# Kernel optimization log

Measured on AMD Instinct MI355X. Metric: run time of the kernel, lower is better.

The kernel has to match this reference:

```python
import jax, jax.numpy as jnp
import numpy as np

B, D_IN, H, D_OUT = 1024, 64, 128, 16


def setup_inputs() -> dict:
    key = jax.random.key(0)
    k0, k1, k2 = jax.random.split(key, 3)
    x = jax.random.normal(k0, (B, D_IN), dtype=jnp.float32)
    W1 = jax.random.normal(k1, (D_IN, H), dtype=jnp.float32) / np.sqrt(D_IN).astype(np.float32)
    b1 = jnp.zeros((H,), dtype=jnp.float32)
    W2 = jax.random.normal(k2, (H, D_OUT), dtype=jnp.float32) / np.sqrt(H).astype(np.float32)
    b2 = jnp.zeros((D_OUT,), dtype=jnp.float32)
    return {"x": x, "W1": W1, "b1": b1, "W2": W2, "b2": b2}


def reference(x, W1, b1, W2, b2):
    # Wrapped net: 2-layer tanh MLP (hessQuik NN equivalent).
    def f_single(xi):  # xi: [D_IN] -> [D_OUT]
        return jnp.tanh(xi @ W1 + b1) @ W2 + b2

    # f: [B, D_OUT]  (torch: f.view(B, -1))
    f = jax.vmap(f_single)(x)

    # Torch builds df[b, i, j] = d f_j / d x_i via one grad per output column;
    # one reverse sweep per output == jacrev, vmapped over batch.
    J = jax.vmap(jax.jacrev(f_single))(x)            # [B, D_OUT, D_IN]
    df = jnp.transpose(J, (0, 2, 1))                 # [B, D_IN, D_OUT]

    # Torch builds d2f[b, k, i, j] = d^2 f_j / (d x_k d x_i); symmetric in (k, i).
    Hs = jax.vmap(jax.hessian(f_single))(x)          # [B, D_OUT, D_IN, D_IN]
    d2f = jnp.transpose(Hs, (0, 2, 3, 1))            # [B, D_IN, D_IN, D_OUT]

    return f, df, d2f
```

## Files before the change

### kernel.cpp

```cpp
#include <hip/hip_runtime.h>
#include <hip/hip_bf16.h>


typedef unsigned short u16;
typedef short s8v __attribute__((ext_vector_type(8)));
typedef float f4v __attribute__((ext_vector_type(4)));

__device__ __forceinline__ u16 f2bf(float f){
  __hip_bfloat16 h = __float2bfloat16(f);
  return __builtin_bit_cast(u16, h);
}

#define W1S 132

__global__ __launch_bounds__(256) void k2_fused(
    const float* __restrict__ x, const float* __restrict__ W1, const float* __restrict__ b1,
    const float* __restrict__ W2, float* __restrict__ d2f)
{
  const int tid  = threadIdx.x;
  const int lane = tid & 63;
  const int wave = tid >> 6;
  const int n = lane & 15;
  const int q = lane >> 4;
  const int b0 = blockIdx.x * 4;
  const int mb = blockIdx.y;

  __shared__ float sW1[64 * W1S];
  __shared__ u16   sG[4 * 2048];
  __shared__ float sx[256];

#pragma unroll
  for (int v = 0; v < 8; ++v){
    int idx = v*256 + tid;
    int r = idx >> 5;
    int c = (idx & 31) << 2;
    *(f4v*)&sW1[r*W1S + c] = *(const f4v*)&W1[r*128 + c];
  }
  sx[tid] = x[b0*64 + tid];
  __syncthreads();

#pragma unroll
  for (int it = 0; it < 2; ++it){
    int idx = it*256 + tid;
    int s = idx >> 7;
    int h = idx & 127;
    float z = b1[h];
#pragma unroll 8
    for (int i = 0; i < 64; ++i) z += sx[s*64 + i] * sW1[i*W1S + h];
    float a = tanhf(z);
    float t = -2.0f * a * (1.0f - a*a);
    f4v w2r[4];
#pragma unroll
    for (int v2 = 0; v2 < 4; ++v2) w2r[v2] = *(const f4v*)&W2[h*16 + v2*4];
#pragma unroll
    for (int j = 0; j < 16; ++j){
      int byte = (j*256 + h*2) ^ ((j & 7) << 4);
      sG[s*2048 + (byte >> 1)] = f2bf(t * w2r[j >> 2][j & 3]);
    }
  }
  __syncthreads();

  s8v bfrag[4][4];
#pragma unroll
  for (int s = 0; s < 4; ++s){
#pragma unroll
    for (int ks = 0; ks < 4; ++ks){
      int byte = (n*256 + q*16 + ks*64) ^ ((n & 7) << 4);
      bfrag[s][ks] = *(const s8v*)&sG[s*2048 + (byte >> 1)];
    }
  }

  const int R0 = mb*2048 + wave*512;
#pragma unroll 2
  for (int mt = 0; mt < 32; ++mt){
    const int rowbase = R0 + mt*16;
    const int r = rowbase + n;
    const int i = r & 63;
    const int k = r >> 6;
    const float* wi = &sW1[i*W1S];
    const float* wk = &sW1[k*W1S];
    s8v afrag[4];
#pragma unroll
    for (int ks = 0; ks < 4; ++ks){
      int c = q*8 + ks*32;
      f4v ia = *(const f4v*)&wi[c];
      f4v ib = *(const f4v*)&wi[c+4];
      f4v ka = *(const f4v*)&wk[c];
      f4v kb = *(const f4v*)&wk[c+4];
      s8v av;
#pragma unroll
      for (int e = 0; e < 4; ++e) av[e]   = (short)f2bf(ia[e]*ka[e]);
#pragma unroll
      for (int e = 0; e < 4; ++e) av[4+e] = (short)f2bf(ib[e]*kb[e]);
      afrag[ks] = av;
    }
#pragma unroll
    for (int s = 0; s < 4; ++s){
      f4v acc = {0.f, 0.f, 0.f, 0.f};
#pragma unroll
      for (int ks = 0; ks < 4; ++ks)
        acc = __builtin_amdgcn_mfma_f32_16x16x32_bf16(bfrag[s][ks], afrag[ks], acc, 0, 0, 0);
      float* op = d2f + (size_t)(b0 + s)*65536 + (size_t)(rowbase + n)*16 + q*4;
      __builtin_nontemporal_store(acc, (f4v*)op);
    }
  }
}

__global__ __launch_bounds__(128) void k1_fdf(
    const float* __restrict__ x,  const float* __restrict__ W1, const float* __restrict__ b1,
    const float* __restrict__ W2, const float* __restrict__ b2,
    float* __restrict__ f_out, float* __restrict__ df_out)
{
  const int b   = blockIdx.x;
  const int tid = threadIdx.x;

  __shared__ float sx[64];
  __shared__ float s_a[128];
  __shared__ float s_sw2[128 * 16];

  if (tid < 64) sx[tid] = x[b*64 + tid];
  __syncthreads();

  float z = b1[tid];
#pragma unroll 8
  for (int i = 0; i < 64; ++i) z += sx[i] * W1[i*128 + tid];
  float a = tanhf(z);
  float s = 1.0f - a*a;
  s_a[tid] = a;
#pragma unroll
  for (int j = 0; j < 16; ++j)
    s_sw2[tid*16 + j] = s * W2[tid*16 + j];
  __syncthreads();

  if (tid < 16){
    float acc = b2[tid];
    for (int h = 0; h < 128; ++h) acc += s_a[h] * W2[h*16 + tid];
    __builtin_nontemporal_store(acc, &f_out[b*16 + tid]);
  }

  const int i  = tid >> 1;
  const int j0 = (tid & 1) * 8;
  float acc[8] = {0,0,0,0,0,0,0,0};
  for (int h0 = 0; h0 < 128; h0 += 8){
    const float4* wp = (const float4*)&W1[i*128 + h0];
    float4 wa = wp[0], wb = wp[1];
    float wf[8] = {wa.x, wa.y, wa.z, wa.w, wb.x, wb.y, wb.z, wb.w};
#pragma unroll
    for (int hh = 0; hh < 8; ++hh){
      const float4* sp = (const float4*)&s_sw2[(h0 + hh)*16 + j0];
      float4 A = sp[0], Bv = sp[1];
      float w1 = wf[hh];
      acc[0] += w1*A.x;  acc[1] += w1*A.y;  acc[2] += w1*A.z;  acc[3] += w1*A.w;
      acc[4] += w1*Bv.x; acc[5] += w1*Bv.y; acc[6] += w1*Bv.z; acc[7] += w1*Bv.w;
    }
  }
  f4v v0 = {acc[0], acc[1], acc[2], acc[3]};
  f4v v1 = {acc[4], acc[5], acc[6], acc[7]};
  float* dp = &df_out[b*1024 + i*16 + j0];
  __builtin_nontemporal_store(v0, (f4v*)dp);
  __builtin_nontemporal_store(v1, (f4v*)(dp + 4));
}

extern "C" void kernel_launch(void* const* d_in, const int* in_sizes, int n_in,
                              void* d_out, int out_size, void* d_ws, size_t ws_size,
                              hipStream_t stream)
{
  (void)in_sizes; (void)n_in; (void)out_size; (void)d_ws; (void)ws_size;
  const float* x  = (const float*)d_in[0];
  const float* W1 = (const float*)d_in[1];
  const float* b1 = (const float*)d_in[2];
  const float* W2 = (const float*)d_in[3];
  const float* b2 = (const float*)d_in[4];

  float* out     = (float*)d_out;
  float* f_out   = out;
  float* df_out  = out + 16384;
  float* d2f_out = out + 1064960;

  k2_fused<<<dim3(256, 2), 256, 0, stream>>>(x, W1, b1, W2, d2f_out);
  k1_fdf<<<1024, 128, 0, stream>>>(x, W1, b1, W2, b2, f_out, df_out);
}
```

Before: 298.9 us.

## Fuse f/df computation into the Hessian kernel and drop the second launch

Merges the separate f/df kernel into the d2f kernel. Each (batch-group, half) block reuses the tanh values it already computed for two of its four samples to produce f and df, staging s*W2 in the now-freed Hessian LDS buffer. This removes one kernel launch and recomputation of the hidden layer. It adds an extra barrier and some serial work before the MFMA store loop. The d2f stores also change from nontemporal to regular stores.

Result: faster. 276.3 us (-7.5%).

```diff
diff --git a/kernel.cpp b/kernel.cpp
--- a/kernel.cpp
+++ b/kernel.cpp
@@ -13,9 +13,10 @@
 
 #define W1S 132
 
-__global__ __launch_bounds__(256) void k2_fused(
+__global__ __launch_bounds__(256) void k_all(
     const float* __restrict__ x, const float* __restrict__ W1, const float* __restrict__ b1,
-    const float* __restrict__ W2, float* __restrict__ d2f)
+    const float* __restrict__ W2, const float* __restrict__ b2,
+    float* __restrict__ f_out, float* __restrict__ df_out, float* __restrict__ d2f)
 {
   const int tid  = threadIdx.x;
   const int lane = tid & 63;
@@ -26,8 +27,9 @@
   const int mb = blockIdx.y;
 
   __shared__ float sW1[64 * W1S];
-  __shared__ u16   sG[4 * 2048];
+  __shared__ __align__(16) float sGF[4096];
   __shared__ float sx[256];
+  u16* sG = (u16*)sGF;
 
 #pragma unroll
   for (int v = 0; v < 8; ++v){
@@ -39,6 +41,7 @@
   sx[tid] = x[b0*64 + tid];
   __syncthreads();
 
+  float a_keep = 0.f, s_keep = 0.f;
 #pragma unroll
   for (int it = 0; it < 2; ++it){
     int idx = it*256 + tid;
@@ -48,7 +51,9 @@
 #pragma unroll 8
     for (int i = 0; i < 64; ++i) z += sx[s*64 + i] * sW1[i*W1S + h];
     float a = tanhf(z);
-    float t = -2.0f * a * (1.0f - a*a);
+    float sd = 1.0f - a*a;
+    float t = -2.0f * a * sd;
+    if (it == mb){ a_keep = a; s_keep = sd; }
     f4v w2r[4];
 #pragma unroll
     for (int v2 = 0; v2 < 4; ++v2) w2r[v2] = *(const f4v*)&W2[h*16 + v2*4];
@@ -67,6 +72,55 @@
     for (int ks = 0; ks < 4; ++ks){
       int byte = (n*256 + q*16 + ks*64) ^ ((n & 7) << 4);
       bfrag[s][ks] = *(const s8v*)&sG[s*2048 + (byte >> 1)];
+    }
+  }
+  __syncthreads();
+
+  {
+    const int ls = tid >> 7;
+    const int h  = tid & 127;
+    float* sF = sGF;
+    sx[tid] = a_keep;
+    f4v w2r[4];
+#pragma unroll
+    for (int v2 = 0; v2 < 4; ++v2) w2r[v2] = *(const f4v*)&W2[h*16 + v2*4];
+#pragma unroll
+    for (int v2 = 0; v2 < 4; ++v2){
+      f4v sv;
+#pragma unroll
+      for (int e = 0; e < 4; ++e) sv[e] = s_keep * w2r[v2][e];
+      *(f4v*)&sF[ls*2048 + h*16 + v2*4] = sv;
+    }
+    __syncthreads();
+
+    const int sub = tid & 127;
+    const int i   = sub >> 1;
+    const int j0  = (sub & 1) * 8;
+    const int bS  = b0 + 2*mb + ls;
+    float acc[8] = {0,0,0,0,0,0,0,0};
+    for (int h0 = 0; h0 < 128; h0 += 8){
+      const float4* wp = (const float4*)&W1[i*128 + h0];
+      float4 wa = wp[0], wb = wp[1];
+      float wf[8] = {wa.x, wa.y, wa.z, wa.w, wb.x, wb.y, wb.z, wb.w};
+#pragma unroll
+      for (int hh = 0; hh < 8; ++hh){
+        const f4v* sp = (const f4v*)&sF[ls*2048 + (h0 + hh)*16 + j0];
+        f4v A = sp[0], Bv = sp[1];
+        float w1 = wf[hh];
+        acc[0] += w1*A[0];  acc[1] += w1*A[1];  acc[2] += w1*A[2];  acc[3] += w1*A[3];
+        acc[4] += w1*Bv[0]; acc[5] += w1*Bv[1]; acc[6] += w1*Bv[2]; acc[7] += w1*Bv[3];
+      }
+    }
+    f4v v0 = {acc[0], acc[1], acc[2], acc[3]};
+    f4v v1 = {acc[4], acc[5], acc[6], acc[7]};
+    float* dp = &df_out[bS*1024 + i*16 + j0];
+    __builtin_nontemporal_store(v0, (f4v*)dp);
+    __builtin_nontemporal_store(v1, (f4v*)(dp + 4));
+
+    if (sub < 16){
+      float accf = b2[sub];
+      for (int h2 = 0; h2 < 128; ++h2) accf += sx[ls*128 + h2] * W2[h2*16 + sub];
+      __builtin_nontemporal_store(accf, &f_out[bS*16 + sub]);
     }
   }
 
@@ -101,64 +155,9 @@
       for (int ks = 0; ks < 4; ++ks)
         acc = __builtin_amdgcn_mfma_f32_16x16x32_bf16(bfrag[s][ks], afrag[ks], acc, 0, 0, 0);
       float* op = d2f + (size_t)(b0 + s)*65536 + (size_t)(rowbase + n)*16 + q*4;
-      __builtin_nontemporal_store(acc, (f4v*)op);
+      *(f4v*)op = acc;
     }
   }
-}
-
-__global__ __launch_bounds__(128) void k1_fdf(
-    const float* __restrict__ x,  const float* __restrict__ W1, const float* __restrict__ b1,
-    const float* __restrict__ W2, const float* __restrict__ b2,
-    float* __restrict__ f_out, float* __restrict__ df_out)
-{
-  const int b   = blockIdx.x;
-  const int tid = threadIdx.x;
-
-  __shared__ float sx[64];
-  __shared__ float s_a[128];
-  __shared__ float s_sw2[128 * 16];
-
-  if (tid < 64) sx[tid] = x[b*64 + tid];
-  __syncthreads();
-
-  float z = b1[tid];
-#pragma unroll 8
-  for (int i = 0; i < 64; ++i) z += sx[i] * W1[i*128 + tid];
-  float a = tanhf(z);
-  float s = 1.0f - a*a;
-  s_a[tid] = a;
-#pragma unroll
-  for (int j = 0; j < 16; ++j)
-    s_sw2[tid*16 + j] = s * W2[tid*16 + j];
-  __syncthreads();
-
-  if (tid < 16){
-    float acc = b2[tid];
-    for (int h = 0; h < 128; ++h) acc += s_a[h] * W2[h*16 + tid];
-    __builtin_nontemporal_store(acc, &f_out[b*16 + tid]);
-  }
-
-  const int i  = tid >> 1;
-  const int j0 = (tid & 1) * 8;
-  float acc[8] = {0,0,0,0,0,0,0,0};
-  for (int h0 = 0; h0 < 128; h0 += 8){
-    const float4* wp = (const float4*)&W1[i*128 + h0];
-    float4 wa = wp[0], wb = wp[1];
-    float wf[8] = {wa.x, wa.y, wa.z, wa.w, wb.x, wb.y, wb.z, wb.w};
-#pragma unroll
-    for (int hh = 0; hh < 8; ++hh){
-      const float4* sp = (const float4*)&s_sw2[(h0 + hh)*16 + j0];
-      float4 A = sp[0], Bv = sp[1];
-      float w1 = wf[hh];
-      acc[0] += w1*A.x;  acc[1] += w1*A.y;  acc[2] += w1*A.z;  acc[3] += w1*A.w;
-      acc[4] += w1*Bv.x; acc[5] += w1*Bv.y; acc[6] += w1*Bv.z; acc[7] += w1*Bv.w;
-    }
-  }
-  f4v v0 = {acc[0], acc[1], acc[2], acc[3]};
-  f4v v1 = {acc[4], acc[5], acc[6], acc[7]};
-  float* dp = &df_out[b*1024 + i*16 + j0];
-  __builtin_nontemporal_store(v0, (f4v*)dp);
-  __builtin_nontemporal_store(v1, (f4v*)(dp + 4));
 }
 
 extern "C" void kernel_launch(void* const* d_in, const int* in_sizes, int n_in,
@@ -177,6 +176,5 @@
   float* df_out  = out + 16384;
   float* d2f_out = out + 1064960;
 
-  k2_fused<<<dim3(256, 2), 256, 0, stream>>>(x, W1, b1, W2, d2f_out);
-  k1_fdf<<<1024, 128, 0, stream>>>(x, W1, b1, W2, b2, f_out, df_out);
+  k_all<<<dim3(256, 2), 256, 0, stream>>>(x, W1, b1, W2, b2, f_out, df_out, d2f_out);
 }
```
